# Kernel optimization log

Measured on AMD Instinct MI355X. Metric: run time of the kernel, lower is better.

The kernel has to match this reference:

```python
import jax, jax.numpy as jnp
import numpy as np

N_NODES = 200000
N_EDGES = 6400000
D_FEAT = 128
N_CLASSES = 40


def setup_inputs() -> dict:
    key = jax.random.key(0)
    ks = jax.random.split(key, 10)
    s_in = 1.0 / np.sqrt(D_FEAT)
    return {
        "x": jax.random.normal(ks[0], (N_NODES, D_FEAT), dtype=jnp.float32),
        "edge_index": jax.random.randint(ks[1], (2, N_EDGES), 0, N_NODES, dtype=jnp.int64),
        "W0": jax.random.normal(ks[2], (D_FEAT, D_FEAT), dtype=jnp.float32) * s_in,
        "b0": jnp.zeros((D_FEAT,), dtype=jnp.float32),
        "W1": jax.random.normal(ks[3], (D_FEAT, D_FEAT), dtype=jnp.float32) * s_in,
        "b1": jnp.zeros((D_FEAT,), dtype=jnp.float32),
        "W2": jax.random.normal(ks[4], (D_FEAT, D_FEAT), dtype=jnp.float32) * s_in,
        "b2": jnp.zeros((D_FEAT,), dtype=jnp.float32),
        "W3": jax.random.normal(ks[5], (D_FEAT, N_CLASSES), dtype=jnp.float32) * s_in,
        "b3": jnp.zeros((N_CLASSES,), dtype=jnp.float32),
    }


def _silu(h):
    return h * jax.nn.sigmoid(h)


def reference(x, edge_index, W0, b0, W1, b1, W2, b2, W3, b3):
    # PyG ChebConv with K=1: out = Tx_0 @ weight[0] + bias, Tx_0 = x.
    # edge_index feeds the scaled-Laplacian norm, which is unused when K == 1.
    del edge_index
    h = _silu(x @ W0 + b0)            # [N, D] ChebConv + SiLU
    h = _silu(h @ W1 + b1)            # [N, D]
    h = _silu(h @ W2 + b2)            # [N, D]
    logits = h @ W3 + b3              # [N, C]
    return jax.nn.log_softmax(logits, axis=1)
```

## Files before the change

### kernel.cpp

```cpp
#include <hip/hip_runtime.h>

#define NN 200000
#define NW 12
#define NBLK 256
#define NT 12500
#define WSTRIDE (NBLK * NW)

typedef __attribute__((ext_vector_type(8))) short bf16x8;
typedef __attribute__((ext_vector_type(4))) float f32x4;
typedef __attribute__((ext_vector_type(4))) unsigned int u32x4;

static __device__ __forceinline__ short f2bf(float f) {
    unsigned u = __builtin_bit_cast(unsigned, f);
    u += 0x7fffu + ((u >> 16) & 1u);
    return (short)(u >> 16);
}

static __device__ __forceinline__ unsigned pk2(float a, float b) {
    unsigned ua = __builtin_bit_cast(unsigned, a) + 0x8000u;
    unsigned ub = __builtin_bit_cast(unsigned, b) + 0x8000u;
    return __builtin_amdgcn_perm(ub, ua, 0x07060302u);
}

static __device__ __forceinline__ int swz(int r, int k) {
    return (r << 7) + (((k >> 3) ^ (r & 15)) << 3) + (k & 7);
}

__global__ void prep_weights_k(const float* __restrict__ W0, const float* __restrict__ W1,
                               const float* __restrict__ W2, const float* __restrict__ W3,
                               short* __restrict__ wt) {
    int e = blockIdx.x * 256 + threadIdx.x;
    if (e < 49152) {
        int l = e >> 14;
        int i = e & 16383;
        int n = i >> 7, k = i & 127;
        const float* W = (l == 0) ? W0 : ((l == 1) ? W1 : W2);
        wt[e] = f2bf(W[(k << 7) + n]);
    } else if (e < 55296) {
        int i = e - 49152;
        int n = i >> 7, k = i & 127;
        wt[e] = (n < 40) ? f2bf(W3[k * 40 + n]) : (short)0;
    }
}

__global__ __launch_bounds__(768)
void mlp_fused_k(const float* __restrict__ x, const short* __restrict__ wt,
                 const float* __restrict__ b0, const float* __restrict__ b1,
                 const float* __restrict__ b2, const float* __restrict__ b3,
                 float* __restrict__ out) {
    __shared__ __align__(16) short sW[55296];
    __shared__ __align__(16) short sA[NW][2048];

    const int tid  = (int)threadIdx.x;
    const int lane = tid & 63;
    const int wv   = tid >> 6;
    const int m    = lane & 15;
    const int quad = lane >> 4;
    short* sAw = &sA[wv][0];

    {
        const u32x4* src = (const u32x4*)wt;
        #pragma unroll
        for (int i = 0; i < 9; ++i) {
            int q = tid + i * 768;
            int R = q >> 4, c = q & 15;
            *(u32x4*)&sW[(R << 7) + ((c ^ (R & 15)) << 3)] = src[q];
        }
    }
    __syncthreads();

    float bv0[8], bv1[8], bv2[8];
    #pragma unroll
    for (int ct = 0; ct < 8; ++ct) {
        bv0[ct] = b0[(ct << 4) + m];
        bv1[ct] = b1[(ct << 4) + m];
        bv2[ct] = b2[(ct << 4) + m];
    }
    const bool val2 = (m < 8);
    float b3v0 = b3[m], b3v1 = b3[16 + m], b3v2 = val2 ? b3[32 + m] : 0.f;

    f32x4 acc[8];
    auto zacc = [&]() {
        #pragma unroll
        for (int ct = 0; ct < 8; ++ct)
            #pragma unroll
            for (int r = 0; r < 4; ++r) acc[ct][r] = 0.f;
    };

    auto epilogue = [&](const float* bv) {
        #pragma unroll
        for (int ct = 0; ct < 8; ++ct)
            #pragma unroll
            for (int r = 0; r < 4; ++r) {
                float v = acc[ct][r] + bv[ct];
                float h = v * __builtin_amdgcn_rcpf(1.f + __expf(-v));
                int rl = (quad << 2) + r;
                unsigned u = __builtin_bit_cast(unsigned, h) + 0x8000u;
                sAw[swz(rl, (ct << 4) + m)] = (short)(u >> 16);
            }
    };

    auto dense = [&](int lbase) {
        zacc();
        #pragma unroll
        for (int ks = 0; ks < 4; ++ks) {
            int kk = (ks << 5) + (quad << 3);
            bf16x8 a0 = *(const bf16x8*)&sAw[swz(m, kk)];
            #pragma unroll
            for (int ct = 0; ct < 8; ++ct) {
                bf16x8 b = *(const bf16x8*)&sW[lbase + swz((ct << 4) + m, kk)];
                acc[ct] = __builtin_amdgcn_mfma_f32_16x16x32_bf16(a0, b, acc[ct], 0, 0, 0);
            }
        }
    };

    int t = (int)blockIdx.x * NW + wv;
    f32x4 xc[8];
    {
        const f32x4* p = (const f32x4*)(x + ((long)(t * 16 + m) << 7)) + quad * 2;
        #pragma unroll
        for (int ks = 0; ks < 4; ++ks) { xc[ks * 2] = p[ks * 8]; xc[ks * 2 + 1] = p[ks * 8 + 1]; }
    }

    while (true) {
        int tn = t + WSTRIDE;
        bool has = tn < NT;
        f32x4 xn[8];
        if (has) {
            const f32x4* p = (const f32x4*)(x + ((long)(tn * 16 + m) << 7)) + quad * 2;
            #pragma unroll
            for (int ks = 0; ks < 4; ++ks) { xn[ks * 2] = p[ks * 8]; xn[ks * 2 + 1] = p[ks * 8 + 1]; }
        }

        zacc();
        #pragma unroll
        for (int ks = 0; ks < 4; ++ks) {
            f32x4 va = xc[ks * 2], vb = xc[ks * 2 + 1];
            u32x4 ua;
            ua[0] = pk2(va[0], va[1]); ua[1] = pk2(va[2], va[3]);
            ua[2] = pk2(vb[0], vb[1]); ua[3] = pk2(vb[2], vb[3]);
            bf16x8 a0 = __builtin_bit_cast(bf16x8, ua);
            int kk = (ks << 5) + (quad << 3);
            #pragma unroll
            for (int ct = 0; ct < 8; ++ct) {
                bf16x8 b = *(const bf16x8*)&sW[swz((ct << 4) + m, kk)];
                acc[ct] = __builtin_amdgcn_mfma_f32_16x16x32_bf16(a0, b, acc[ct], 0, 0, 0);
            }
        }
        epilogue(bv0);
        dense(16384);
        epilogue(bv1);
        dense(32768);
        epilogue(bv2);

        f32x4 c3[3];
        #pragma unroll
        for (int ct = 0; ct < 3; ++ct)
            #pragma unroll
            for (int r = 0; r < 4; ++r) c3[ct][r] = 0.f;
        #pragma unroll
        for (int ks = 0; ks < 4; ++ks) {
            int kk = (ks << 5) + (quad << 3);
            bf16x8 a0 = *(const bf16x8*)&sAw[swz(m, kk)];
            #pragma unroll
            for (int ct = 0; ct < 3; ++ct) {
                bf16x8 b = *(const bf16x8*)&sW[49152 + swz((ct << 4) + m, kk)];
                c3[ct] = __builtin_amdgcn_mfma_f32_16x16x32_bf16(a0, b, c3[ct], 0, 0, 0);
            }
        }
        #pragma unroll
        for (int r = 0; r < 4; ++r) {
            float v0 = c3[0][r] + b3v0;
            float v1 = c3[1][r] + b3v1;
            float v2 = c3[2][r] + b3v2;
            float mx = fmaxf(v0, v1);
            mx = val2 ? fmaxf(mx, v2) : mx;
            #pragma unroll
            for (int s = 1; s < 16; s <<= 1)
                mx = fmaxf(mx, __shfl_xor(mx, s, 64));
            float sm = __expf(v0 - mx) + __expf(v1 - mx) + (val2 ? __expf(v2 - mx) : 0.f);
            #pragma unroll
            for (int s = 1; s < 16; s <<= 1)
                sm += __shfl_xor(sm, s, 64);
            float L = mx + __logf(sm);
            int grow = t * 16 + (quad << 2) + r;
            float* orow = out + (long)grow * 40;
            orow[m]      = v0 - L;
            orow[16 + m] = v1 - L;
            if (val2) orow[32 + m] = v2 - L;
        }

        if (!has) break;
        #pragma unroll
        for (int i = 0; i < 8; ++i) xc[i] = xn[i];
        t = tn;
    }
}

extern "C" void kernel_launch(void* const* d_in, const int* in_sizes, int n_in,
                              void* d_out, int out_size, void* d_ws, size_t ws_size,
                              hipStream_t stream) {
    const float* x   = (const float*)d_in[0];
    const float* W0  = (const float*)d_in[2];
    const float* bb0 = (const float*)d_in[3];
    const float* W1  = (const float*)d_in[4];
    const float* bb1 = (const float*)d_in[5];
    const float* W2  = (const float*)d_in[6];
    const float* bb2 = (const float*)d_in[7];
    const float* W3  = (const float*)d_in[8];
    const float* bb3 = (const float*)d_in[9];
    short* wt  = (short*)d_ws;
    float* out = (float*)d_out;

    hipLaunchKernelGGL(prep_weights_k, dim3(216), dim3(256), 0, stream, W0, W1, W2, W3, wt);
    hipLaunchKernelGGL(mlp_fused_k, dim3(NBLK), dim3(768), 0, stream,
                       x, wt, bb0, bb1, bb2, bb3, out);
}
```

Measured before the change: 230.4 us.

## Use atomic work-stealing tickets for tile scheduling and trim prefetch registers

Static strided tile assignment per wave is replaced by a global atomic ticket counter, so each wave grabs its next 16-row tile dynamically. The x input is converted to bf16 before the next tile is prefetched, which lets one register buffer be reused instead of keeping separate current and next arrays. The final layer's accumulators reuse the acc array, and launch bounds request 3 waves per SIMD to limit register use. The aim is to balance load across waves and lower register pressure, at the cost of one atomic per tile and an extra memset launch.

```diff
diff --git a/kernel.cpp b/kernel.cpp
--- a/kernel.cpp
+++ b/kernel.cpp
@@ -5,6 +5,7 @@
 #define NBLK 256
 #define NT 12500
 #define WSTRIDE (NBLK * NW)
+#define CNT_OFF 110592
 
 typedef __attribute__((ext_vector_type(8))) short bf16x8;
 typedef __attribute__((ext_vector_type(4))) float f32x4;
@@ -43,11 +44,11 @@
     }
 }
 
-__global__ __launch_bounds__(768)
+__global__ __launch_bounds__(768, 3)
 void mlp_fused_k(const float* __restrict__ x, const short* __restrict__ wt,
                  const float* __restrict__ b0, const float* __restrict__ b1,
                  const float* __restrict__ b2, const float* __restrict__ b3,
-                 float* __restrict__ out) {
+                 unsigned* __restrict__ ticket, float* __restrict__ out) {
     __shared__ __align__(16) short sW[55296];
     __shared__ __align__(16) short sA[NW][2048];
 
@@ -115,36 +116,42 @@
     };
 
     int t = (int)blockIdx.x * NW + wv;
-    f32x4 xc[8];
+    f32x4 xr[8];
     {
         const f32x4* p = (const f32x4*)(x + ((long)(t * 16 + m) << 7)) + quad * 2;
         #pragma unroll
-        for (int ks = 0; ks < 4; ++ks) { xc[ks * 2] = p[ks * 8]; xc[ks * 2 + 1] = p[ks * 8 + 1]; }
+        for (int ks = 0; ks < 4; ++ks) { xr[ks * 2] = p[ks * 8]; xr[ks * 2 + 1] = p[ks * 8 + 1]; }
     }
 
     while (true) {
-        int tn = t + WSTRIDE;
-        bool has = tn < NT;
-        f32x4 xn[8];
-        if (has) {
-            const f32x4* p = (const f32x4*)(x + ((long)(tn * 16 + m) << 7)) + quad * 2;
-            #pragma unroll
-            for (int ks = 0; ks < 4; ++ks) { xn[ks * 2] = p[ks * 8]; xn[ks * 2 + 1] = p[ks * 8 + 1]; }
-        }
-
-        zacc();
-        #pragma unroll
-        for (int ks = 0; ks < 4; ++ks) {
-            f32x4 va = xc[ks * 2], vb = xc[ks * 2 + 1];
+        bf16x8 ab[4];
+        #pragma unroll
+        for (int ks = 0; ks < 4; ++ks) {
+            f32x4 va = xr[ks * 2], vb = xr[ks * 2 + 1];
             u32x4 ua;
             ua[0] = pk2(va[0], va[1]); ua[1] = pk2(va[2], va[3]);
             ua[2] = pk2(vb[0], vb[1]); ua[3] = pk2(vb[2], vb[3]);
-            bf16x8 a0 = __builtin_bit_cast(bf16x8, ua);
+            ab[ks] = __builtin_bit_cast(bf16x8, ua);
+        }
+
+        int tn;
+        if (lane == 0) tn = WSTRIDE + (int)atomicAdd(ticket, 1u);
+        tn = __shfl(tn, 0, 64);
+        bool has = tn < NT;
+        if (has) {
+            const f32x4* p = (const f32x4*)(x + ((long)(tn * 16 + m) << 7)) + quad * 2;
+            #pragma unroll
+            for (int ks = 0; ks < 4; ++ks) { xr[ks * 2] = p[ks * 8]; xr[ks * 2 + 1] = p[ks * 8 + 1]; }
+        }
+
+        zacc();
+        #pragma unroll
+        for (int ks = 0; ks < 4; ++ks) {
             int kk = (ks << 5) + (quad << 3);
             #pragma unroll
             for (int ct = 0; ct < 8; ++ct) {
                 bf16x8 b = *(const bf16x8*)&sW[swz((ct << 4) + m, kk)];
-                acc[ct] = __builtin_amdgcn_mfma_f32_16x16x32_bf16(a0, b, acc[ct], 0, 0, 0);
+                acc[ct] = __builtin_amdgcn_mfma_f32_16x16x32_bf16(ab[ks], b, acc[ct], 0, 0, 0);
             }
         }
         epilogue(bv0);
@@ -153,11 +160,10 @@
         dense(32768);
         epilogue(bv2);
 
-        f32x4 c3[3];
         #pragma unroll
         for (int ct = 0; ct < 3; ++ct)
             #pragma unroll
-            for (int r = 0; r < 4; ++r) c3[ct][r] = 0.f;
+            for (int r = 0; r < 4; ++r) acc[ct][r] = 0.f;
         #pragma unroll
         for (int ks = 0; ks < 4; ++ks) {
             int kk = (ks << 5) + (quad << 3);
@@ -165,14 +171,14 @@
             #pragma unroll
             for (int ct = 0; ct < 3; ++ct) {
                 bf16x8 b = *(const bf16x8*)&sW[49152 + swz((ct << 4) + m, kk)];
-                c3[ct] = __builtin_amdgcn_mfma_f32_16x16x32_bf16(a0, b, c3[ct], 0, 0, 0);
+                acc[ct] = __builtin_amdgcn_mfma_f32_16x16x32_bf16(a0, b, acc[ct], 0, 0, 0);
             }
         }
         #pragma unroll
         for (int r = 0; r < 4; ++r) {
-            float v0 = c3[0][r] + b3v0;
-            float v1 = c3[1][r] + b3v1;
-            float v2 = c3[2][r] + b3v2;
+            float v0 = acc[0][r] + b3v0;
+            float v1 = acc[1][r] + b3v1;
+            float v2 = acc[2][r] + b3v2;
             float mx = fmaxf(v0, v1);
             mx = val2 ? fmaxf(mx, v2) : mx;
             #pragma unroll
@@ -191,8 +197,6 @@
         }
 
         if (!has) break;
-        #pragma unroll
-        for (int i = 0; i < 8; ++i) xc[i] = xn[i];
         t = tn;
     }
 }
@@ -209,10 +213,12 @@
     const float* bb2 = (const float*)d_in[7];
     const float* W3  = (const float*)d_in[8];
     const float* bb3 = (const float*)d_in[9];
-    short* wt  = (short*)d_ws;
-    float* out = (float*)d_out;
-
+    short* wt       = (short*)d_ws;
+    unsigned* cnt   = (unsigned*)((char*)d_ws + CNT_OFF);
+    float* out      = (float*)d_out;
+
+    hipMemsetAsync(cnt, 0, sizeof(unsigned), stream);
     hipLaunchKernelGGL(prep_weights_k, dim3(216), dim3(256), 0, stream, W0, W1, W2, W3, wt);
     hipLaunchKernelGGL(mlp_fused_k, dim3(NBLK), dim3(768), 0, stream,
-                       x, wt, bb0, bb1, bb2, bb3, out);
-}
+                       x, wt, bb0, bb1, bb2, bb3, cnt, out);
+}
```

New measurement: 320.4 us. 39.0% more time.
